# Optimization experiments

Hardware: AMD Instinct MI355X
Metric: run time of the kernel (lower is better)

The kernel has to match this reference:

```python
import jax, jax.numpy as jnp
import numpy as np

N = 4_194_304  # total points
C = 2          # classes: 0=ground, 1=plant
B = 8          # number of point clouds in the batch
SIGMA_L = 0.1
SIGMA_R = 0.4
CLAMP_FACTOR = 2.0
MIN_VAL = 0.1
FOCAL_GAMMA = 2.0
FOCAL_ALPHA = 1.0
LOSS_WEIGHT = 1.0


def setup_inputs() -> dict:
    key = jax.random.key(0)
    k1, k2, k3 = jax.random.split(key, 3)
    pred = jax.random.normal(k1, (N, C), dtype=jnp.float32)
    coord = jax.random.normal(k2, (N, 3), dtype=jnp.float32)
    segment = jax.random.randint(k3, (N,), 0, C, dtype=jnp.int32)
    # pointcept-style cumulative offsets: equal-sized clouds, offset[-1] == N
    offset = (jnp.arange(1, B + 1, dtype=jnp.int32) * (N // B))
    return {"pred": pred, "coord": coord, "segment": segment, "offset": offset}


def _gauss_weights(z, segment, batch):
    # per-cloud z_ground_max (fallback: z.min) and z_plant_min (fallback: z.max)
    neg_inf = jnp.array(-jnp.inf, z.dtype)
    pos_inf = jnp.array(jnp.inf, z.dtype)
    gmax = jax.ops.segment_max(jnp.where(segment == 0, z, neg_inf), batch, num_segments=B)
    pmin = jax.ops.segment_min(jnp.where(segment == 1, z, pos_inf), batch, num_segments=B)
    has_g = jax.ops.segment_sum((segment == 0).astype(z.dtype), batch, num_segments=B) > 0
    has_p = jax.ops.segment_sum((segment == 1).astype(z.dtype), batch, num_segments=B) > 0
    zmin = jax.ops.segment_min(z, batch, num_segments=B)
    zmax = jax.ops.segment_max(z, batch, num_segments=B)
    g = jnp.where(has_g, gmax, zmin)
    p = jnp.where(has_p, pmin, zmax)
    mu_b = g + (p - g) * 0.5  # (B,)
    mu = mu_b[batch]          # (N,)
    d = z - mu
    w_left = jnp.exp(-(d * d) / (2.0 * SIGMA_L * SIGMA_L))
    w_right = jnp.exp(-(d * d) / (2.0 * SIGMA_R * SIGMA_R))
    w_right = jnp.where(d > CLAMP_FACTOR * SIGMA_R, jnp.array(MIN_VAL, z.dtype), w_right)
    return jnp.where(z <= mu, w_left, w_right)


def reference(pred, coord, segment, offset):
    n = pred.shape[0]
    # offset2batch: per-point batch id from cumulative offsets
    batch = jnp.searchsorted(offset, jnp.arange(n, dtype=offset.dtype), side='right')
    # cross entropy (reduction='none')
    logp = jax.nn.log_softmax(pred, axis=1)              # (N, C)
    logp_t = jnp.take_along_axis(logp, segment[:, None], axis=1)[:, 0]  # (N,)
    seg_loss = (-logp_t) * LOSS_WEIGHT
    # focal reweighting (computed under no_grad in the original)
    p_t = jax.lax.stop_gradient(jnp.exp(logp_t))
    focal_weight = FOCAL_ALPHA * (1.0 - p_t) ** FOCAL_GAMMA
    seg_loss = seg_loss * focal_weight
    # asymmetric gaussian z-weighting, segment-conditioned per cloud
    weights = _gauss_weights(coord[:, 2], segment, batch)
    return jnp.mean(seg_loss * weights)
```

## Files before the change

### kernel.cpp

```cpp
#include <hip/hip_runtime.h>
#include <math.h>

#define THREADS 1024
#define NBLOCKS 256
#define UNROLL  8

__device__ __forceinline__ unsigned enc_f(float f) {
    unsigned b = __float_as_uint(f);
    return (b & 0x80000000u) ? ~b : (b | 0x80000000u);
}
__device__ __forceinline__ float dec_f(unsigned u) {
    unsigned b = (u & 0x80000000u) ? (u ^ 0x80000000u) : ~u;
    return __uint_as_float(b);
}
#define ENC_NEG_INF 0x007FFFFFu
#define ENC_POS_INF 0xFF800000u
__device__ __forceinline__ unsigned ident_w(int w) {
    return (w < 8 || w >= 24) ? ENC_NEG_INF : ENC_POS_INF;
}

#define SLOT(base, blk) ((base) + 64 + (blk) * 32)

#define CNT_B(ii, bdst) do { bdst = 0; \
    _Pragma("unroll") for (int j_ = 0; j_ < 8; ++j_) bdst += ((ii) >= roff[j_]); } while (0)

#define FLUSH_LDS(bb, g_, p_, mn_, mx_) do { \
    atomicMax(&s_stats[      (bb)], enc_f(g_));  \
    atomicMin(&s_stats[ 8  + (bb)], enc_f(p_));  \
    atomicMin(&s_stats[16  + (bb)], enc_f(mn_)); \
    atomicMax(&s_stats[24  + (bb)], enc_f(mx_)); } while (0)

__global__ __launch_bounds__(THREADS) void k_stats(
        const float* __restrict__ coord, const int* __restrict__ segment,
        const int* __restrict__ offset, unsigned* __restrict__ ws, int n, int nb) {
    __shared__ unsigned s_stats[32];
    const int tid = threadIdx.x;
    if (tid < 32) s_stats[tid] = ident_w(tid);
    if (blockIdx.x == 0 && tid == THREADS - 1) {
        *(double*)(ws + 32) = 0.0;
        ws[34] = 0u;
    }
    int roff[8];
    #pragma unroll
    for (int j = 0; j < 8; ++j) roff[j] = (j < nb) ? offset[j] : 0x7FFFFFFF;
    __syncthreads();

    const int chunk = (n + (int)gridDim.x - 1) / (int)gridDim.x;
    const int start = blockIdx.x * chunk;
    const int end   = min(n, start + chunk);

    float lg = -INFINITY, lp = INFINITY, lmn = INFINITY, lmx = -INFINITY;

    if (start < end) {
        int ba = 0, bb = 0;
        #pragma unroll
        for (int j = 0; j < 8; ++j) { ba += (start >= roff[j]); bb += ((end - 1) >= roff[j]); }
        if (ba == bb) {
            int i = start + tid;
            for (; i + (UNROLL - 1) * THREADS < end; i += UNROLL * THREADS) {
                float z[UNROLL]; int s[UNROLL];
                #pragma unroll
                for (int k = 0; k < UNROLL; ++k) z[k] = coord[3 * (i + k * THREADS) + 2];
                #pragma unroll
                for (int k = 0; k < UNROLL; ++k) s[k] = segment[i + k * THREADS];
                #pragma unroll
                for (int k = 0; k < UNROLL; ++k) {
                    lmn = fminf(lmn, z[k]);
                    lmx = fmaxf(lmx, z[k]);
                    lg  = fmaxf(lg, (s[k] == 0) ? z[k] : -INFINITY);
                    lp  = fminf(lp, (s[k] != 0) ? z[k] : INFINITY);
                }
            }
            for (; i < end; i += THREADS) {
                float z = coord[3 * i + 2]; int s = segment[i];
                lmn = fminf(lmn, z); lmx = fmaxf(lmx, z);
                lg  = fmaxf(lg, (s == 0) ? z : -INFINITY);
                lp  = fminf(lp, (s != 0) ? z : INFINITY);
            }
            #pragma unroll
            for (int m = 32; m; m >>= 1) {
                lg  = fmaxf(lg,  __shfl_xor(lg,  m, 64));
                lp  = fminf(lp,  __shfl_xor(lp,  m, 64));
                lmn = fminf(lmn, __shfl_xor(lmn, m, 64));
                lmx = fmaxf(lmx, __shfl_xor(lmx, m, 64));
            }
            if ((tid & 63) == 0) FLUSH_LDS(ba, lg, lp, lmn, lmx);
        } else {
            int curb = -1;
            for (int i = start + tid; i < end; i += THREADS) {
                float z = coord[3 * i + 2]; int s = segment[i], b;
                CNT_B(i, b);
                if (b != curb) {
                    if (curb >= 0) FLUSH_LDS(curb, lg, lp, lmn, lmx);
                    lg = -INFINITY; lp = INFINITY; lmn = INFINITY; lmx = -INFINITY;
                    curb = b;
                }
                lmn = fminf(lmn, z); lmx = fmaxf(lmx, z);
                if (s == 0) lg = fmaxf(lg, z); else lp = fminf(lp, z);
            }
            if (curb >= 0) FLUSH_LDS(curb, lg, lp, lmn, lmx);
        }
    }
    __syncthreads();
    if (tid < 32) SLOT(ws, blockIdx.x)[tid] = s_stats[tid];
}

__device__ __forceinline__ float point_loss(float p0, float p1, int s, float z, float mu) {
    float m   = fmaxf(p0, p1);
    float lse = m + logf(expf(p0 - m) + expf(p1 - m));
    float lpt = ((s == 0) ? p0 : p1) - lse;
    float pt  = expf(lpt);
    float om  = 1.0f - pt;
    float loss = -lpt * om * om;
    float d  = z - mu;
    float cf = (z <= mu) ? 50.0f : 3.125f;
    float w  = expf(-d * d * cf);
    if (z > mu && d > 0.8f) w = 0.1f;
    return loss * w;
}

__global__ __launch_bounds__(THREADS) void k_loss(
        const float* __restrict__ pred, const float* __restrict__ coord,
        const int* __restrict__ segment, const int* __restrict__ offset,
        unsigned* __restrict__ ws, float* __restrict__ out, int n, int nb) {
    __shared__ unsigned s_comb[32];
    __shared__ float    s_mu[8];
    __shared__ float    s_part[THREADS / 64];
    const int tid = threadIdx.x;
    int roff[8];
    #pragma unroll
    for (int j = 0; j < 8; ++j) roff[j] = (j < nb) ? offset[j] : 0x7FFFFFFF;

    if (tid < 32) s_comb[tid] = ident_w(tid);
    __syncthreads();
    {
        const int w = tid & 31, g = tid >> 5;
        unsigned v = ident_w(w);
        #pragma unroll
        for (int j = 0; j < NBLOCKS / 32; ++j) {
            unsigned u = SLOT((const unsigned*)ws, g * (NBLOCKS / 32) + j)[w];
            v = (w < 8 || w >= 24) ? max(v, u) : min(v, u);
        }
        if (w < 8 || w >= 24) atomicMax(&s_comb[w], v);
        else                  atomicMin(&s_comb[w], v);
    }
    __syncthreads();
    if (tid < 8) {
        unsigned ug = s_comb[tid], up = s_comb[8 + tid];
        float g = dec_f(ug), p = dec_f(up);
        if (ug == ENC_NEG_INF) g = dec_f(s_comb[16 + tid]);
        if (up == ENC_POS_INF) p = dec_f(s_comb[24 + tid]);
        s_mu[tid] = g + (p - g) * 0.5f;
    }
    __syncthreads();

    const int chunk = (n + (int)gridDim.x - 1) / (int)gridDim.x;
    const int start = blockIdx.x * chunk;
    const int end   = min(n, start + chunk);
    const float2* pred2 = (const float2*)pred;

    float lsum = 0.0f;
    if (start < end) {
        int ba = 0, bb = 0;
        #pragma unroll
        for (int j = 0; j < 8; ++j) { ba += (start >= roff[j]); bb += ((end - 1) >= roff[j]); }
        if (ba == bb) {
            const float mu = s_mu[ba];
            int i = start + tid;
            for (; i + (UNROLL - 1) * THREADS < end; i += UNROLL * THREADS) {
                float z[UNROLL]; int s[UNROLL]; float2 pp[UNROLL];
                #pragma unroll
                for (int k = 0; k < UNROLL; ++k) pp[k] = pred2[i + k * THREADS];
                #pragma unroll
                for (int k = 0; k < UNROLL; ++k) z[k] = coord[3 * (i + k * THREADS) + 2];
                #pragma unroll
                for (int k = 0; k < UNROLL; ++k) s[k] = segment[i + k * THREADS];
                #pragma unroll
                for (int k = 0; k < UNROLL; ++k)
                    lsum += point_loss(pp[k].x, pp[k].y, s[k], z[k], mu);
            }
            for (; i < end; i += THREADS) {
                float2 pp = pred2[i];
                lsum += point_loss(pp.x, pp.y, segment[i], coord[3 * i + 2], mu);
            }
        } else {
            for (int i = start + tid; i < end; i += THREADS) {
                int b; CNT_B(i, b);
                float2 pp = pred2[i];
                lsum += point_loss(pp.x, pp.y, segment[i], coord[3 * i + 2], s_mu[b]);
            }
        }
    }

    #pragma unroll
    for (int off = 32; off > 0; off >>= 1) lsum += __shfl_down(lsum, off, 64);
    if ((tid & 63) == 0) s_part[tid >> 6] = lsum;
    __syncthreads();
    if (tid == 0) {
        float t = 0.0f;
        #pragma unroll
        for (int wv = 0; wv < THREADS / 64; ++wv) t += s_part[wv];
        double* acc = (double*)(ws + 32);
        atomicAdd(acc, (double)t);
        __threadfence();
        unsigned c = atomicAdd(&ws[34], 1u);
        if (c == (unsigned)gridDim.x - 1u) {
            double v = atomicAdd(acc, 0.0);
            out[0] = (float)(v / (double)n);
        }
    }
}

extern "C" void kernel_launch(void* const* d_in, const int* in_sizes, int n_in,
                              void* d_out, int out_size, void* d_ws, size_t ws_size,
                              hipStream_t stream) {
    const float* pred    = (const float*)d_in[0];
    const float* coord   = (const float*)d_in[1];
    const int*   segment = (const int*)d_in[2];
    const int*   offset  = (const int*)d_in[3];
    const int n  = in_sizes[2];
    const int nb = in_sizes[3];

    unsigned* ws = (unsigned*)d_ws;

    hipLaunchKernelGGL(k_stats, dim3(NBLOCKS), dim3(THREADS), 0, stream,
                       coord, segment, offset, ws, n, nb);
    hipLaunchKernelGGL(k_loss,  dim3(NBLOCKS), dim3(THREADS), 0, stream,
                       pred, coord, segment, offset, ws, (float*)d_out, n, nb);
}
```

Baseline: 132.9 us.

## Fuse stats and loss passes into one cooperative kernel with register-cached z and segment

Merges the two kernels into a single cooperative launch that computes the per-cloud statistics, syncs the whole grid, then computes the loss. The first 16 z values per thread are held in registers and the segment labels are packed into a bitmask, so the loss phase reads only pred for those elements and does not reload coord and segment. This removes one kernel launch and most of the second pass over coord and segment, but adds a grid-wide barrier and more register pressure. The 16K-element chunk per block means the cache covers the whole chunk for this input size.

New measurement: 221.9 us. 1.67x slower.

```diff
diff --git a/kernel.cpp b/kernel.cpp
--- a/kernel.cpp
+++ b/kernel.cpp
@@ -1,9 +1,12 @@
 #include <hip/hip_runtime.h>
+#include <hip/hip_cooperative_groups.h>
 #include <math.h>
+
+namespace cg = cooperative_groups;
 
 #define THREADS 1024
 #define NBLOCKS 256
-#define UNROLL  8
+#define CACHE_K 16
 
 __device__ __forceinline__ unsigned enc_f(float f) {
     unsigned b = __float_as_uint(f);
@@ -29,81 +32,6 @@
     atomicMin(&s_stats[ 8  + (bb)], enc_f(p_));  \
     atomicMin(&s_stats[16  + (bb)], enc_f(mn_)); \
     atomicMax(&s_stats[24  + (bb)], enc_f(mx_)); } while (0)
-
-__global__ __launch_bounds__(THREADS) void k_stats(
-        const float* __restrict__ coord, const int* __restrict__ segment,
-        const int* __restrict__ offset, unsigned* __restrict__ ws, int n, int nb) {
-    __shared__ unsigned s_stats[32];
-    const int tid = threadIdx.x;
-    if (tid < 32) s_stats[tid] = ident_w(tid);
-    if (blockIdx.x == 0 && tid == THREADS - 1) {
-        *(double*)(ws + 32) = 0.0;
-        ws[34] = 0u;
-    }
-    int roff[8];
-    #pragma unroll
-    for (int j = 0; j < 8; ++j) roff[j] = (j < nb) ? offset[j] : 0x7FFFFFFF;
-    __syncthreads();
-
-    const int chunk = (n + (int)gridDim.x - 1) / (int)gridDim.x;
-    const int start = blockIdx.x * chunk;
-    const int end   = min(n, start + chunk);
-
-    float lg = -INFINITY, lp = INFINITY, lmn = INFINITY, lmx = -INFINITY;
-
-    if (start < end) {
-        int ba = 0, bb = 0;
-        #pragma unroll
-        for (int j = 0; j < 8; ++j) { ba += (start >= roff[j]); bb += ((end - 1) >= roff[j]); }
-        if (ba == bb) {
-            int i = start + tid;
-            for (; i + (UNROLL - 1) * THREADS < end; i += UNROLL * THREADS) {
-                float z[UNROLL]; int s[UNROLL];
-                #pragma unroll
-                for (int k = 0; k < UNROLL; ++k) z[k] = coord[3 * (i + k * THREADS) + 2];
-                #pragma unroll
-                for (int k = 0; k < UNROLL; ++k) s[k] = segment[i + k * THREADS];
-                #pragma unroll
-                for (int k = 0; k < UNROLL; ++k) {
-                    lmn = fminf(lmn, z[k]);
-                    lmx = fmaxf(lmx, z[k]);
-                    lg  = fmaxf(lg, (s[k] == 0) ? z[k] : -INFINITY);
-                    lp  = fminf(lp, (s[k] != 0) ? z[k] : INFINITY);
-                }
-            }
-            for (; i < end; i += THREADS) {
-                float z = coord[3 * i + 2]; int s = segment[i];
-                lmn = fminf(lmn, z); lmx = fmaxf(lmx, z);
-                lg  = fmaxf(lg, (s == 0) ? z : -INFINITY);
-                lp  = fminf(lp, (s != 0) ? z : INFINITY);
-            }
-            #pragma unroll
-            for (int m = 32; m; m >>= 1) {
-                lg  = fmaxf(lg,  __shfl_xor(lg,  m, 64));
-                lp  = fminf(lp,  __shfl_xor(lp,  m, 64));
-                lmn = fminf(lmn, __shfl_xor(lmn, m, 64));
-                lmx = fmaxf(lmx, __shfl_xor(lmx, m, 64));
-            }
-            if ((tid & 63) == 0) FLUSH_LDS(ba, lg, lp, lmn, lmx);
-        } else {
-            int curb = -1;
-            for (int i = start + tid; i < end; i += THREADS) {
-                float z = coord[3 * i + 2]; int s = segment[i], b;
-                CNT_B(i, b);
-                if (b != curb) {
-                    if (curb >= 0) FLUSH_LDS(curb, lg, lp, lmn, lmx);
-                    lg = -INFINITY; lp = INFINITY; lmn = INFINITY; lmx = -INFINITY;
-                    curb = b;
-                }
-                lmn = fminf(lmn, z); lmx = fmaxf(lmx, z);
-                if (s == 0) lg = fmaxf(lg, z); else lp = fminf(lp, z);
-            }
-            if (curb >= 0) FLUSH_LDS(curb, lg, lp, lmn, lmx);
-        }
-    }
-    __syncthreads();
-    if (tid < 32) SLOT(ws, blockIdx.x)[tid] = s_stats[tid];
-}
 
 __device__ __forceinline__ float point_loss(float p0, float p1, int s, float z, float mu) {
     float m   = fmaxf(p0, p1);
@@ -119,17 +47,116 @@
     return loss * w;
 }
 
-__global__ __launch_bounds__(THREADS) void k_loss(
+__global__ __launch_bounds__(THREADS, 4) void k_fused(
         const float* __restrict__ pred, const float* __restrict__ coord,
         const int* __restrict__ segment, const int* __restrict__ offset,
         unsigned* __restrict__ ws, float* __restrict__ out, int n, int nb) {
+    __shared__ unsigned s_stats[32];
     __shared__ unsigned s_comb[32];
     __shared__ float    s_mu[8];
     __shared__ float    s_part[THREADS / 64];
     const int tid = threadIdx.x;
+
+    if (tid < 32) s_stats[tid] = ident_w(tid);
+    if (blockIdx.x == 0 && tid == THREADS - 1) {
+        atomicExch((unsigned long long*)(ws + 32), 0ull);
+        atomicExch(&ws[34], 0u);
+    }
     int roff[8];
     #pragma unroll
     for (int j = 0; j < 8; ++j) roff[j] = (j < nb) ? offset[j] : 0x7FFFFFFF;
+    __syncthreads();
+
+    const int chunk = (n + (int)gridDim.x - 1) / (int)gridDim.x;
+    const int start = blockIdx.x * chunk;
+    const int end   = min(n, start + chunk);
+
+    float    zc[CACHE_K];
+    unsigned segbits = 0u;
+    int  ba = 0, bb = 0;
+    bool fast = false;
+    float lg = -INFINITY, lp = INFINITY, lmn = INFINITY, lmx = -INFINITY;
+
+    if (start < end) {
+        #pragma unroll
+        for (int j = 0; j < 8; ++j) { ba += (start >= roff[j]); bb += ((end - 1) >= roff[j]); }
+        fast = (ba == bb);
+        if (fast) {
+            #pragma unroll
+            for (int k = 0; k < CACHE_K; ++k) {
+                int i = start + tid + k * THREADS;
+                zc[k] = (i < end) ? coord[3 * i + 2] : 0.0f;
+            }
+            int sv[CACHE_K];
+            #pragma unroll
+            for (int k = 0; k < CACHE_K; ++k) {
+                int i = start + tid + k * THREADS;
+                sv[k] = (i < end) ? segment[i] : 0;
+            }
+            #pragma unroll
+            for (int k = 0; k < CACHE_K; ++k) {
+                int i = start + tid + k * THREADS;
+                segbits |= (unsigned)(sv[k] & 1) << k;
+                if (i < end) {
+                    float z = zc[k];
+                    lmn = fminf(lmn, z); lmx = fmaxf(lmx, z);
+                    lg  = fmaxf(lg, (sv[k] == 0) ? z : -INFINITY);
+                    lp  = fminf(lp, (sv[k] != 0) ? z : INFINITY);
+                }
+            }
+            for (int i = start + tid + CACHE_K * THREADS; i < end; i += THREADS) {
+                float z = coord[3 * i + 2]; int s = segment[i];
+                lmn = fminf(lmn, z); lmx = fmaxf(lmx, z);
+                lg  = fmaxf(lg, (s == 0) ? z : -INFINITY);
+                lp  = fminf(lp, (s != 0) ? z : INFINITY);
+            }
+            #pragma unroll
+            for (int m = 32; m; m >>= 1) {
+                lg  = fmaxf(lg,  __shfl_xor(lg,  m, 64));
+                lp  = fminf(lp,  __shfl_xor(lp,  m, 64));
+                lmn = fminf(lmn, __shfl_xor(lmn, m, 64));
+                lmx = fmaxf(lmx, __shfl_xor(lmx, m, 64));
+            }
+            if ((tid & 63) == 0) FLUSH_LDS(ba, lg, lp, lmn, lmx);
+        } else {
+            int curb = -1;
+            #pragma unroll
+            for (int k = 0; k < CACHE_K; ++k) {
+                int i = start + tid + k * THREADS;
+                bool ok = (i < end);
+                float z = ok ? coord[3 * i + 2] : 0.0f;
+                int   s = ok ? segment[i] : 0;
+                zc[k] = z;
+                segbits |= (unsigned)(s & 1) << k;
+                if (ok) {
+                    int b; CNT_B(i, b);
+                    if (b != curb) {
+                        if (curb >= 0) FLUSH_LDS(curb, lg, lp, lmn, lmx);
+                        lg = -INFINITY; lp = INFINITY; lmn = INFINITY; lmx = -INFINITY;
+                        curb = b;
+                    }
+                    lmn = fminf(lmn, z); lmx = fmaxf(lmx, z);
+                    if (s == 0) lg = fmaxf(lg, z); else lp = fminf(lp, z);
+                }
+            }
+            for (int i = start + tid + CACHE_K * THREADS; i < end; i += THREADS) {
+                float z = coord[3 * i + 2]; int s = segment[i], b;
+                CNT_B(i, b);
+                if (b != curb) {
+                    if (curb >= 0) FLUSH_LDS(curb, lg, lp, lmn, lmx);
+                    lg = -INFINITY; lp = INFINITY; lmn = INFINITY; lmx = -INFINITY;
+                    curb = b;
+                }
+                lmn = fminf(lmn, z); lmx = fmaxf(lmx, z);
+                if (s == 0) lg = fmaxf(lg, z); else lp = fminf(lp, z);
+            }
+            if (curb >= 0) FLUSH_LDS(curb, lg, lp, lmn, lmx);
+        }
+    }
+    __syncthreads();
+    if (tid < 32) SLOT(ws, blockIdx.x)[tid] = s_stats[tid];
+    __threadfence();
+    cg::this_grid().sync();
 
     if (tid < 32) s_comb[tid] = ident_w(tid);
     __syncthreads();
@@ -154,37 +181,45 @@
     }
     __syncthreads();
 
-    const int chunk = (n + (int)gridDim.x - 1) / (int)gridDim.x;
-    const int start = blockIdx.x * chunk;
-    const int end   = min(n, start + chunk);
     const float2* pred2 = (const float2*)pred;
-
     float lsum = 0.0f;
     if (start < end) {
-        int ba = 0, bb = 0;
-        #pragma unroll
-        for (int j = 0; j < 8; ++j) { ba += (start >= roff[j]); bb += ((end - 1) >= roff[j]); }
-        if (ba == bb) {
+        if (fast) {
             const float mu = s_mu[ba];
-            int i = start + tid;
-            for (; i + (UNROLL - 1) * THREADS < end; i += UNROLL * THREADS) {
-                float z[UNROLL]; int s[UNROLL]; float2 pp[UNROLL];
+            const int ibase = start + tid;
+            #pragma unroll
+            for (int k0 = 0; k0 < CACHE_K; k0 += 8) {
+                float2 pp[8];
                 #pragma unroll
-                for (int k = 0; k < UNROLL; ++k) pp[k] = pred2[i + k * THREADS];
+                for (int kk = 0; kk < 8; ++kk) {
+                    int i = ibase + (k0 + kk) * THREADS;
+                    pp[kk] = (i < end) ? pred2[i] : make_float2(0.0f, 0.0f);
+                }
                 #pragma unroll
-                for (int k = 0; k < UNROLL; ++k) z[k] = coord[3 * (i + k * THREADS) + 2];
-                #pragma unroll
-                for (int k = 0; k < UNROLL; ++k) s[k] = segment[i + k * THREADS];
-                #pragma unroll
-                for (int k = 0; k < UNROLL; ++k)
-                    lsum += point_loss(pp[k].x, pp[k].y, s[k], z[k], mu);
-            }
-            for (; i < end; i += THREADS) {
+                for (int kk = 0; kk < 8; ++kk) {
+                    int i = ibase + (k0 + kk) * THREADS;
+                    if (i < end)
+                        lsum += point_loss(pp[kk].x, pp[kk].y,
+                                           (int)((segbits >> (k0 + kk)) & 1u),
+                                           zc[k0 + kk], mu);
+                }
+            }
+            for (int i = ibase + CACHE_K * THREADS; i < end; i += THREADS) {
                 float2 pp = pred2[i];
                 lsum += point_loss(pp.x, pp.y, segment[i], coord[3 * i + 2], mu);
             }
         } else {
-            for (int i = start + tid; i < end; i += THREADS) {
+            #pragma unroll
+            for (int k = 0; k < CACHE_K; ++k) {
+                int i = start + tid + k * THREADS;
+                if (i < end) {
+                    int b; CNT_B(i, b);
+                    float2 pp = pred2[i];
+                    lsum += point_loss(pp.x, pp.y, (int)((segbits >> k) & 1u),
+                                       zc[k], s_mu[b]);
+                }
+            }
+            for (int i = start + tid + CACHE_K * THREADS; i < end; i += THREADS) {
                 int b; CNT_B(i, b);
                 float2 pp = pred2[i];
                 lsum += point_loss(pp.x, pp.y, segment[i], coord[3 * i + 2], s_mu[b]);
@@ -218,13 +253,13 @@
     const float* coord   = (const float*)d_in[1];
     const int*   segment = (const int*)d_in[2];
     const int*   offset  = (const int*)d_in[3];
-    const int n  = in_sizes[2];
-    const int nb = in_sizes[3];
-
+    int n  = in_sizes[2];
+    int nb = in_sizes[3];
     unsigned* ws = (unsigned*)d_ws;
-
-    hipLaunchKernelGGL(k_stats, dim3(NBLOCKS), dim3(THREADS), 0, stream,
-                       coord, segment, offset, ws, n, nb);
-    hipLaunchKernelGGL(k_loss,  dim3(NBLOCKS), dim3(THREADS), 0, stream,
-                       pred, coord, segment, offset, ws, (float*)d_out, n, nb);
-}
+    float* out = (float*)d_out;
+
+    void* args[] = { (void*)&pred, (void*)&coord, (void*)&segment, (void*)&offset,
+                     (void*)&ws, (void*)&out, (void*)&n, (void*)&nb };
+    hipLaunchCooperativeKernel((void*)k_fused, dim3(NBLOCKS), dim3(THREADS),
+                               args, 0, stream);
+}
```

## Compact z and segment bytes in stats pass, reuse them in loss pass

Applied to the files above, without the earlier changes.

The stats kernel now reads coord and segment as vectorized float4/int4 and writes a compacted z array plus byte-packed segment labels into workspace. The loss kernel reads only pred, the compact z and the packed labels, avoiding strided coord re-reads and full int segment reads. The cross-block reduction of mu moves into a separate single-block kernel, and grid and block sizes change. The cost is an extra 20 MB of writes, an extra launch, and reliance on a workspace large enough for the new offsets.

Measured after the change: 184.8 us. +39.0%, slower.

```diff
diff --git a/kernel.cpp b/kernel.cpp
--- a/kernel.cpp
+++ b/kernel.cpp
@@ -1,9 +1,10 @@
 #include <hip/hip_runtime.h>
 #include <math.h>
 
-#define THREADS 1024
-#define NBLOCKS 256
-#define UNROLL  8
+#define TS  1024
+#define NBS 512
+#define TL  512
+#define NBL 1024
 
 __device__ __forceinline__ unsigned enc_f(float f) {
     unsigned b = __float_as_uint(f);
@@ -20,6 +21,8 @@
 }
 
 #define SLOT(base, blk) ((base) + 64 + (blk) * 32)
+#define ZOFF_W (1u << 20)
+#define SOFF_W (8u << 20)
 
 #define CNT_B(ii, bdst) do { bdst = 0; \
     _Pragma("unroll") for (int j_ = 0; j_ < 8; ++j_) bdst += ((ii) >= roff[j_]); } while (0)
@@ -29,81 +32,6 @@
     atomicMin(&s_stats[ 8  + (bb)], enc_f(p_));  \
     atomicMin(&s_stats[16  + (bb)], enc_f(mn_)); \
     atomicMax(&s_stats[24  + (bb)], enc_f(mx_)); } while (0)
-
-__global__ __launch_bounds__(THREADS) void k_stats(
-        const float* __restrict__ coord, const int* __restrict__ segment,
-        const int* __restrict__ offset, unsigned* __restrict__ ws, int n, int nb) {
-    __shared__ unsigned s_stats[32];
-    const int tid = threadIdx.x;
-    if (tid < 32) s_stats[tid] = ident_w(tid);
-    if (blockIdx.x == 0 && tid == THREADS - 1) {
-        *(double*)(ws + 32) = 0.0;
-        ws[34] = 0u;
-    }
-    int roff[8];
-    #pragma unroll
-    for (int j = 0; j < 8; ++j) roff[j] = (j < nb) ? offset[j] : 0x7FFFFFFF;
-    __syncthreads();
-
-    const int chunk = (n + (int)gridDim.x - 1) / (int)gridDim.x;
-    const int start = blockIdx.x * chunk;
-    const int end   = min(n, start + chunk);
-
-    float lg = -INFINITY, lp = INFINITY, lmn = INFINITY, lmx = -INFINITY;
-
-    if (start < end) {
-        int ba = 0, bb = 0;
-        #pragma unroll
-        for (int j = 0; j < 8; ++j) { ba += (start >= roff[j]); bb += ((end - 1) >= roff[j]); }
-        if (ba == bb) {
-            int i = start + tid;
-            for (; i + (UNROLL - 1) * THREADS < end; i += UNROLL * THREADS) {
-                float z[UNROLL]; int s[UNROLL];
-                #pragma unroll
-                for (int k = 0; k < UNROLL; ++k) z[k] = coord[3 * (i + k * THREADS) + 2];
-                #pragma unroll
-                for (int k = 0; k < UNROLL; ++k) s[k] = segment[i + k * THREADS];
-                #pragma unroll
-                for (int k = 0; k < UNROLL; ++k) {
-                    lmn = fminf(lmn, z[k]);
-                    lmx = fmaxf(lmx, z[k]);
-                    lg  = fmaxf(lg, (s[k] == 0) ? z[k] : -INFINITY);
-                    lp  = fminf(lp, (s[k] != 0) ? z[k] : INFINITY);
-                }
-            }
-            for (; i < end; i += THREADS) {
-                float z = coord[3 * i + 2]; int s = segment[i];
-                lmn = fminf(lmn, z); lmx = fmaxf(lmx, z);
-                lg  = fmaxf(lg, (s == 0) ? z : -INFINITY);
-                lp  = fminf(lp, (s != 0) ? z : INFINITY);
-            }
-            #pragma unroll
-            for (int m = 32; m; m >>= 1) {
-                lg  = fmaxf(lg,  __shfl_xor(lg,  m, 64));
-                lp  = fminf(lp,  __shfl_xor(lp,  m, 64));
-                lmn = fminf(lmn, __shfl_xor(lmn, m, 64));
-                lmx = fmaxf(lmx, __shfl_xor(lmx, m, 64));
-            }
-            if ((tid & 63) == 0) FLUSH_LDS(ba, lg, lp, lmn, lmx);
-        } else {
-            int curb = -1;
-            for (int i = start + tid; i < end; i += THREADS) {
-                float z = coord[3 * i + 2]; int s = segment[i], b;
-                CNT_B(i, b);
-                if (b != curb) {
-                    if (curb >= 0) FLUSH_LDS(curb, lg, lp, lmn, lmx);
-                    lg = -INFINITY; lp = INFINITY; lmn = INFINITY; lmx = -INFINITY;
-                    curb = b;
-                }
-                lmn = fminf(lmn, z); lmx = fmaxf(lmx, z);
-                if (s == 0) lg = fmaxf(lg, z); else lp = fminf(lp, z);
-            }
-            if (curb >= 0) FLUSH_LDS(curb, lg, lp, lmn, lmx);
-        }
-    }
-    __syncthreads();
-    if (tid < 32) SLOT(ws, blockIdx.x)[tid] = s_stats[tid];
-}
 
 __device__ __forceinline__ float point_loss(float p0, float p1, int s, float z, float mu) {
     float m   = fmaxf(p0, p1);
@@ -119,75 +47,159 @@
     return loss * w;
 }
 
-__global__ __launch_bounds__(THREADS) void k_loss(
-        const float* __restrict__ pred, const float* __restrict__ coord,
-        const int* __restrict__ segment, const int* __restrict__ offset,
+__global__ __launch_bounds__(TS, 8) void k_stats(
+        const float* __restrict__ coord, const int* __restrict__ segment,
+        const int* __restrict__ offset, unsigned* __restrict__ ws, int n, int nb) {
+    __shared__ unsigned s_stats[32];
+    const int tid = threadIdx.x;
+    if (tid < 32) s_stats[tid] = ident_w(tid);
+    int roff[8];
+    #pragma unroll
+    for (int j = 0; j < 8; ++j) roff[j] = (j < nb) ? offset[j] : 0x7FFFFFFF;
+    __syncthreads();
+
+    int chunk = (n + (int)gridDim.x - 1) / (int)gridDim.x;
+    chunk = (chunk + 3) & ~3;
+    const int start = blockIdx.x * chunk;
+    const int end   = min(n, start + chunk);
+
+    float*         zs = (float*)(ws + ZOFF_W);
+    unsigned char* sb = (unsigned char*)(ws + SOFF_W);
+
+    if (start < end) {
+        int ba = 0, bb = 0;
+        #pragma unroll
+        for (int j = 0; j < 8; ++j) { ba += (start >= roff[j]); bb += ((end - 1) >= roff[j]); }
+        float lg = -INFINITY, lp = INFINITY, lmn = INFINITY, lmx = -INFINITY;
+
+        if (ba == bb && ((end - start) % (4 * TS) == 0)) {
+            const float4* c4 = (const float4*)coord;
+            const int4*   s4 = (const int4*)segment;
+            float4*       z4 = (float4*)zs;
+            unsigned*     sw = (unsigned*)sb;
+            for (int p0 = start; p0 < end; p0 += 4 * TS) {
+                const int q = (p0 >> 2) + tid;
+                float4 a = c4[3 * q + 0];
+                float4 b = c4[3 * q + 1];
+                float4 c = c4[3 * q + 2];
+                int4   s = s4[q];
+                const float z0 = a.z, z1 = b.y, z2 = c.x, z3 = c.w;
+                z4[q] = make_float4(z0, z1, z2, z3);
+                sw[q] = (unsigned)(s.x & 1) | ((unsigned)(s.y & 1) << 8)
+                      | ((unsigned)(s.z & 1) << 16) | ((unsigned)(s.w & 1) << 24);
+                lmn = fminf(lmn, fminf(fminf(z0, z1), fminf(z2, z3)));
+                lmx = fmaxf(lmx, fmaxf(fmaxf(z0, z1), fmaxf(z2, z3)));
+                lg = fmaxf(lg, (s.x == 0) ? z0 : -INFINITY);
+                lg = fmaxf(lg, (s.y == 0) ? z1 : -INFINITY);
+                lg = fmaxf(lg, (s.z == 0) ? z2 : -INFINITY);
+                lg = fmaxf(lg, (s.w == 0) ? z3 : -INFINITY);
+                lp = fminf(lp, (s.x != 0) ? z0 : INFINITY);
+                lp = fminf(lp, (s.y != 0) ? z1 : INFINITY);
+                lp = fminf(lp, (s.z != 0) ? z2 : INFINITY);
+                lp = fminf(lp, (s.w != 0) ? z3 : INFINITY);
+            }
+            #pragma unroll
+            for (int m = 32; m; m >>= 1) {
+                lg  = fmaxf(lg,  __shfl_xor(lg,  m, 64));
+                lp  = fminf(lp,  __shfl_xor(lp,  m, 64));
+                lmn = fminf(lmn, __shfl_xor(lmn, m, 64));
+                lmx = fmaxf(lmx, __shfl_xor(lmx, m, 64));
+            }
+            if ((tid & 63) == 0) FLUSH_LDS(ba, lg, lp, lmn, lmx);
+        } else {
+            int curb = -1;
+            for (int i = start + tid; i < end; i += TS) {
+                float z = coord[3 * i + 2]; int s = segment[i], b;
+                zs[i] = z;
+                sb[i] = (unsigned char)(s & 1);
+                CNT_B(i, b);
+                if (b != curb) {
+                    if (curb >= 0) FLUSH_LDS(curb, lg, lp, lmn, lmx);
+                    lg = -INFINITY; lp = INFINITY; lmn = INFINITY; lmx = -INFINITY;
+                    curb = b;
+                }
+                lmn = fminf(lmn, z); lmx = fmaxf(lmx, z);
+                if (s == 0) lg = fmaxf(lg, z); else lp = fminf(lp, z);
+            }
+            if (curb >= 0) FLUSH_LDS(curb, lg, lp, lmn, lmx);
+        }
+    }
+    __syncthreads();
+    if (tid < 32) SLOT(ws, blockIdx.x)[tid] = s_stats[tid];
+}
+
+__global__ __launch_bounds__(256) void k_mu(unsigned* __restrict__ ws) {
+    __shared__ unsigned s_comb[32];
+    const int tid = threadIdx.x;
+    if (tid < 32) s_comb[tid] = ident_w(tid);
+    __syncthreads();
+    const int w = tid & 31, g = tid >> 5;
+    unsigned v = ident_w(w);
+    for (int j = g; j < NBS; j += 8) {
+        unsigned u = SLOT((const unsigned*)ws, j)[w];
+        v = (w < 8 || w >= 24) ? max(v, u) : min(v, u);
+    }
+    if (w < 8 || w >= 24) atomicMax(&s_comb[w], v);
+    else                  atomicMin(&s_comb[w], v);
+    __syncthreads();
+    if (tid < 8) {
+        unsigned ug = s_comb[tid], up = s_comb[8 + tid];
+        float gv = dec_f(ug), pv = dec_f(up);
+        if (ug == ENC_NEG_INF) gv = dec_f(s_comb[16 + tid]);
+        if (up == ENC_POS_INF) pv = dec_f(s_comb[24 + tid]);
+        ws[40 + tid] = __float_as_uint(gv + (pv - gv) * 0.5f);
+    }
+    if (tid == 64) { *(double*)(ws + 32) = 0.0; ws[35] = 0u; }
+}
+
+__global__ __launch_bounds__(TL, 8) void k_loss(
+        const float* __restrict__ pred, const int* __restrict__ offset,
         unsigned* __restrict__ ws, float* __restrict__ out, int n, int nb) {
-    __shared__ unsigned s_comb[32];
-    __shared__ float    s_mu[8];
-    __shared__ float    s_part[THREADS / 64];
+    __shared__ float s_mu[8];
+    __shared__ float s_part[TL / 64];
     const int tid = threadIdx.x;
     int roff[8];
     #pragma unroll
     for (int j = 0; j < 8; ++j) roff[j] = (j < nb) ? offset[j] : 0x7FFFFFFF;
-
-    if (tid < 32) s_comb[tid] = ident_w(tid);
-    __syncthreads();
-    {
-        const int w = tid & 31, g = tid >> 5;
-        unsigned v = ident_w(w);
-        #pragma unroll
-        for (int j = 0; j < NBLOCKS / 32; ++j) {
-            unsigned u = SLOT((const unsigned*)ws, g * (NBLOCKS / 32) + j)[w];
-            v = (w < 8 || w >= 24) ? max(v, u) : min(v, u);
-        }
-        if (w < 8 || w >= 24) atomicMax(&s_comb[w], v);
-        else                  atomicMin(&s_comb[w], v);
-    }
-    __syncthreads();
-    if (tid < 8) {
-        unsigned ug = s_comb[tid], up = s_comb[8 + tid];
-        float g = dec_f(ug), p = dec_f(up);
-        if (ug == ENC_NEG_INF) g = dec_f(s_comb[16 + tid]);
-        if (up == ENC_POS_INF) p = dec_f(s_comb[24 + tid]);
-        s_mu[tid] = g + (p - g) * 0.5f;
-    }
-    __syncthreads();
-
-    const int chunk = (n + (int)gridDim.x - 1) / (int)gridDim.x;
+    if (tid < 8) s_mu[tid] = __uint_as_float(ws[40 + tid]);
+    __syncthreads();
+
+    int chunk = (n + (int)gridDim.x - 1) / (int)gridDim.x;
+    chunk = (chunk + 3) & ~3;
     const int start = blockIdx.x * chunk;
     const int end   = min(n, start + chunk);
-    const float2* pred2 = (const float2*)pred;
+
+    const float*         zs  = (const float*)(ws + ZOFF_W);
+    const unsigned char* sbB = (const unsigned char*)(ws + SOFF_W);
 
     float lsum = 0.0f;
     if (start < end) {
         int ba = 0, bb = 0;
         #pragma unroll
         for (int j = 0; j < 8; ++j) { ba += (start >= roff[j]); bb += ((end - 1) >= roff[j]); }
-        if (ba == bb) {
+
+        if (ba == bb && ((end - start) % (4 * TL) == 0)) {
             const float mu = s_mu[ba];
-            int i = start + tid;
-            for (; i + (UNROLL - 1) * THREADS < end; i += UNROLL * THREADS) {
-                float z[UNROLL]; int s[UNROLL]; float2 pp[UNROLL];
-                #pragma unroll
-                for (int k = 0; k < UNROLL; ++k) pp[k] = pred2[i + k * THREADS];
-                #pragma unroll
-                for (int k = 0; k < UNROLL; ++k) z[k] = coord[3 * (i + k * THREADS) + 2];
-                #pragma unroll
-                for (int k = 0; k < UNROLL; ++k) s[k] = segment[i + k * THREADS];
-                #pragma unroll
-                for (int k = 0; k < UNROLL; ++k)
-                    lsum += point_loss(pp[k].x, pp[k].y, s[k], z[k], mu);
-            }
-            for (; i < end; i += THREADS) {
-                float2 pp = pred2[i];
-                lsum += point_loss(pp.x, pp.y, segment[i], coord[3 * i + 2], mu);
+            const float4*   p4 = (const float4*)pred;
+            const float4*   z4 = (const float4*)zs;
+            const unsigned* sw = (const unsigned*)sbB;
+            for (int p0 = start; p0 < end; p0 += 4 * TL) {
+                const int q = (p0 >> 2) + tid;
+                float4 pa = p4[2 * q + 0];
+                float4 pb = p4[2 * q + 1];
+                float4 zz = z4[q];
+                unsigned s = sw[q];
+                lsum += point_loss(pa.x, pa.y, (int)( s        & 1u), zz.x, mu);
+                lsum += point_loss(pa.z, pa.w, (int)((s >>  8) & 1u), zz.y, mu);
+                lsum += point_loss(pb.x, pb.y, (int)((s >> 16) & 1u), zz.z, mu);
+                lsum += point_loss(pb.z, pb.w, (int)((s >> 24) & 1u), zz.w, mu);
             }
         } else {
-            for (int i = start + tid; i < end; i += THREADS) {
+            const float2* pred2 = (const float2*)pred;
+            for (int i = start + tid; i < end; i += TL) {
                 int b; CNT_B(i, b);
                 float2 pp = pred2[i];
-                lsum += point_loss(pp.x, pp.y, segment[i], coord[3 * i + 2], s_mu[b]);
+                lsum += point_loss(pp.x, pp.y, (int)sbB[i], zs[i], s_mu[b]);
             }
         }
     }
@@ -199,11 +211,11 @@
     if (tid == 0) {
         float t = 0.0f;
         #pragma unroll
-        for (int wv = 0; wv < THREADS / 64; ++wv) t += s_part[wv];
+        for (int wv = 0; wv < TL / 64; ++wv) t += s_part[wv];
         double* acc = (double*)(ws + 32);
         atomicAdd(acc, (double)t);
         __threadfence();
-        unsigned c = atomicAdd(&ws[34], 1u);
+        unsigned c = atomicAdd(&ws[35], 1u);
         if (c == (unsigned)gridDim.x - 1u) {
             double v = atomicAdd(acc, 0.0);
             out[0] = (float)(v / (double)n);
@@ -220,11 +232,11 @@
     const int*   offset  = (const int*)d_in[3];
     const int n  = in_sizes[2];
     const int nb = in_sizes[3];
-
     unsigned* ws = (unsigned*)d_ws;
 
-    hipLaunchKernelGGL(k_stats, dim3(NBLOCKS), dim3(THREADS), 0, stream,
+    hipLaunchKernelGGL(k_stats, dim3(NBS), dim3(TS), 0, stream,
                        coord, segment, offset, ws, n, nb);
-    hipLaunchKernelGGL(k_loss,  dim3(NBLOCKS), dim3(THREADS), 0, stream,
-                       pred, coord, segment, offset, ws, (float*)d_out, n, nb);
-}
+    hipLaunchKernelGGL(k_mu, dim3(1), dim3(256), 0, stream, ws);
+    hipLaunchKernelGGL(k_loss, dim3(NBL), dim3(TL), 0, stream,
+                       pred, offset, ws, (float*)d_out, n, nb);
+}
```
